# Kernel optimization log

Hardware: AMD Instinct MI355X
Metric: run time of the kernel (lower is better)

The kernel has to match this reference:

```python
import jax, jax.numpy as jnp
import numpy as np

B, C, H, W = 8, 512, 32, 32
NH, DH = 8, 64          # num_heads, head_dim (C = NH*DH)
GROUPS, EPS = 32, 1e-5


def group_norm(x, gamma, beta):
    b, c, h, w = x.shape
    xg = x.reshape(b, GROUPS, c // GROUPS, h, w)
    mu = xg.mean(axis=(2, 3, 4), keepdims=True)
    var = xg.var(axis=(2, 3, 4), keepdims=True)
    xn = ((xg - mu) * jax.lax.rsqrt(var + EPS)).reshape(b, c, h, w)
    return xn * gamma[:, None, None] + beta[:, None, None]


def conv1x1(x, w, b):
    # x: [B,C,H,W], w: [O,C], b: [O]
    return jnp.einsum('bchw,oc->bohw', x, w) + b[:, None, None]


def setup_inputs() -> dict:
    key = jax.random.key(0)
    ks = jax.random.split(key, 5)
    return {
        'x': jax.random.normal(ks[0], (B, C, H, W), jnp.float32),
        'norm_gamma': jnp.ones((C,), jnp.float32),
        'norm_beta': jnp.zeros((C,), jnp.float32),
        'qkv_w': jax.random.normal(ks[1], (3 * C, C), jnp.float32) * (1.0 / np.sqrt(C)),
        'qkv_b': jax.random.normal(ks[2], (3 * C,), jnp.float32) * 0.02,
        'proj_w': jax.random.normal(ks[3], (C, C), jnp.float32) * (1.0 / np.sqrt(C)),
        'proj_b': jax.random.normal(ks[4], (C,), jnp.float32) * 0.02,
    }


def reference(x, norm_gamma, norm_beta, qkv_w, qkv_b, proj_w, proj_b):
    scale = DH ** -0.5
    h = group_norm(x, norm_gamma, norm_beta)
    qkv = conv1x1(h, qkv_w, qkv_b)                       # [B,3C,H,W]
    qkv = qkv.reshape(B, 3, NH, DH, H * W)
    qkv = jnp.transpose(qkv, (1, 0, 2, 4, 3))            # [3,B,NH,HW,DH]
    q, k, v = qkv[0], qkv[1], qkv[2]
    attn = jnp.einsum('bhid,bhjd->bhij', q, k) * scale   # [B,NH,HW,HW]
    attn = jax.nn.softmax(attn, axis=-1)
    h = jnp.einsum('bhij,bhjd->bhid', attn, v)           # [B,NH,HW,DH]
    # faithful to torch: direct row-major reshape [B,NH,HW,DH] -> [B,C,H,W]
    h = h.reshape(B, C, H, W)
    h = conv1x1(h, proj_w, proj_b)
    return x + h
```

## Files before the change

### kernel.cpp

```cpp
#include <hip/hip_runtime.h>


typedef float  f32x4  __attribute__((ext_vector_type(4)));
typedef __bf16 bf16x8 __attribute__((ext_vector_type(8)));
typedef __bf16 bf16x4 __attribute__((ext_vector_type(4)));
typedef short  s16x4  __attribute__((ext_vector_type(4)));

#define MFMA(a, b, c) __builtin_amdgcn_mfma_f32_16x16x32_bf16(a, b, c, 0, 0, 0)
#define MFMA16(a, b, c) __builtin_amdgcn_mfma_f32_16x16x16bf16_1k( \
    __builtin_bit_cast(s16x4, a), __builtin_bit_cast(s16x4, b), c, 0, 0, 0)

__device__ __forceinline__ void async16(const __bf16* g, __bf16* l) {
  __builtin_amdgcn_global_load_lds((const __attribute__((address_space(1))) void*)g,
                                   (__attribute__((address_space(3))) void*)l, 16, 0, 0);
}

__device__ __forceinline__ int chk(int n, int c) {
  return ((((n >> 6) * 16 + (c >> 5)) * 4 + ((c >> 3) & 3)) * 512) + (n & 63) * 8 + (c & 7);
}

__global__ __launch_bounds__(512) void gn_cvt_k(const float* __restrict__ x,
                                                const float* __restrict__ gamma,
                                                const float* __restrict__ beta,
                                                __bf16* __restrict__ Hout,
                                                const float* __restrict__ qw, __bf16* __restrict__ dq,
                                                const float* __restrict__ pw, __bf16* __restrict__ dp) {
  const int tid = threadIdx.x;
  if (blockIdx.x >= 256) {
    int i = ((blockIdx.x - 256) * 512 + tid) * 4;
    const float* src = (i < 786432) ? qw : pw;
    __bf16* dst = (i < 786432) ? dq : dp;
    int j = (i < 786432) ? i : (i - 786432);
    int m = j >> 9, k = j & 511;
    float4 v = *(const float4*)(src + j);
    bf16x4 o;
    o[0] = (__bf16)v.x; o[1] = (__bf16)v.y; o[2] = (__bf16)v.z; o[3] = (__bf16)v.w;
    *(bf16x4*)(dst + chk(m, k)) = o;
    return;
  }
  __shared__ __bf16 xs[16 * 1032];
  __shared__ float  red[16];
  __shared__ float  ga[16], be[16], stat[2];
  const int w = tid >> 6, l = tid & 63;
  const int bg = blockIdx.x, b = bg >> 5, g = bg & 31, c0 = g * 16;
  const float* xg = x + b * 524288 + c0 * 1024;

  float sum = 0.f, sq = 0.f;
#pragma unroll
  for (int p = 0; p < 8; p++) {
    int idx = p * 2048 + tid * 4;
    float4 v = *(const float4*)(xg + idx);
    int c = idx >> 10, s = idx & 1023;
    bf16x4 o;
    o[0] = (__bf16)v.x; o[1] = (__bf16)v.y; o[2] = (__bf16)v.z; o[3] = (__bf16)v.w;
    *(bf16x4*)(&xs[c * 1032 + s]) = o;
    sum += v.x + v.y + v.z + v.w;
    sq  += v.x * v.x + v.y * v.y + v.z * v.z + v.w * v.w;
  }
#pragma unroll
  for (int o = 32; o > 0; o >>= 1) { sum += __shfl_down(sum, o); sq += __shfl_down(sq, o); }
  if (l == 0) { red[w * 2] = sum; red[w * 2 + 1] = sq; }
  __syncthreads();
  if (tid == 0) {
    float S = 0.f, Q = 0.f;
#pragma unroll
    for (int i = 0; i < 8; i++) { S += red[i * 2]; Q += red[i * 2 + 1]; }
    float mean = S * (1.f / 16384.f);
    float var  = Q * (1.f / 16384.f) - mean * mean;
    stat[0] = mean; stat[1] = rsqrtf(var + 1e-5f);
  }
  if (tid < 16) { ga[tid] = gamma[c0 + tid]; be[tid] = beta[c0 + tid]; }
  __syncthreads();
  const float mean = stat[0], rstd = stat[1];
#pragma unroll
  for (int p = 0; p < 2; p++) {
    int s = p * 512 + tid;
    int n = b * 1024 + s;
    bf16x8 o0, o1;
#pragma unroll
    for (int c = 0; c < 8; c++) {
      float f = (float)xs[c * 1032 + s];
      o0[c] = (__bf16)((f - mean) * rstd * ga[c] + be[c]);
    }
#pragma unroll
    for (int c = 8; c < 16; c++) {
      float f = (float)xs[c * 1032 + s];
      o1[c - 8] = (__bf16)((f - mean) * rstd * ga[c] + be[c]);
    }
    *(bf16x8*)(Hout + chk(n, c0)) = o0;
    *(bf16x8*)(Hout + chk(n, c0 + 8)) = o1;
  }
}

__global__ __launch_bounds__(256) void gemm_qkv_k(const __bf16* __restrict__ W,
                                                  const float* __restrict__ bias,
                                                  const __bf16* __restrict__ H,
                                                  __bf16* __restrict__ qbuf,
                                                  __bf16* __restrict__ kbuf,
                                                  __bf16* __restrict__ vt) {
  __shared__ union {
    struct { __bf16 a[2][4096]; __bf16 b[2][4096]; } ab;
    __bf16 cs[128 * 136];
  } lds;
  const int tid = threadIdx.x;
  const int w = tid >> 6, l = tid & 63, quad = l >> 4, li = l & 15;
  const int wr = w >> 1, wc = w & 1;
  const int mblk = blockIdx.x >> 6, nblk = blockIdx.x & 63;
  const int m0 = mblk * 128, n0 = nblk * 128;

  f32x4 acc[4][4];
#pragma unroll
  for (int i = 0; i < 4; i++)
#pragma unroll
    for (int j = 0; j < 4; j++) acc[i][j] = f32x4{0.f, 0.f, 0.f, 0.f};

  const __bf16* Ag = W + (((m0 >> 6) * 16) * 4 + w) * 512 + l * 8;
  const __bf16* Bg = H + (((n0 >> 6) * 16) * 4 + w) * 512 + l * 8;
  const int halfA = 16 * 4 * 512;

  async16(Ag,         &lds.ab.a[0][w * 1024]);
  async16(Ag + halfA, &lds.ab.a[0][w * 1024 + 512]);
  async16(Bg,         &lds.ab.b[0][w * 1024]);
  async16(Bg + halfA, &lds.ab.b[0][w * 1024 + 512]);

#pragma unroll 1
  for (int kt = 0; kt < 16; kt++) {
    int cur = kt & 1, nxt = cur ^ 1;
    __syncthreads();
    if (kt < 15) {
      int ko = (kt + 1) * 2048;
      async16(Ag + ko,          &lds.ab.a[nxt][w * 1024]);
      async16(Ag + halfA + ko,  &lds.ab.a[nxt][w * 1024 + 512]);
      async16(Bg + ko,          &lds.ab.b[nxt][w * 1024]);
      async16(Bg + halfA + ko,  &lds.ab.b[nxt][w * 1024 + 512]);
    }
    bf16x8 af[4], bfr[4];
#pragma unroll
    for (int i = 0; i < 4; i++)
      af[i] = *(const bf16x8*)(&lds.ab.a[cur][quad * 1024 + (wr * 64 + i * 16 + li) * 8]);
#pragma unroll
    for (int i = 0; i < 4; i++)
      bfr[i] = *(const bf16x8*)(&lds.ab.b[cur][quad * 1024 + (wc * 64 + i * 16 + li) * 8]);
#pragma unroll
    for (int i = 0; i < 4; i++)
#pragma unroll
      for (int j = 0; j < 4; j++) acc[i][j] = MFMA(af[i], bfr[j], acc[i][j]);
  }

  const int t = m0 >> 9;
  const int cbase = m0 & 511;
  __syncthreads();
#pragma unroll
  for (int mi = 0; mi < 4; mi++) {
    int olocal = wr * 64 + mi * 16 + quad * 4;
    float bs[4];
#pragma unroll
    for (int r = 0; r < 4; r++) bs[r] = bias[m0 + olocal + r];
#pragma unroll
    for (int ni = 0; ni < 4; ni++) {
      int nlocal = wc * 64 + ni * 16 + li;
      bf16x4 pk;
#pragma unroll
      for (int r = 0; r < 4; r++) {
        float f = acc[mi][ni][r] + bs[r];
        if (t == 0) f *= 0.180336880f;
        pk[r] = (__bf16)f;
      }
      *(bf16x4*)(&lds.cs[nlocal * 136 + olocal]) = pk;
    }
  }
  __syncthreads();
  const int bb = n0 >> 10, s0 = n0 & 1023;
  if (t < 2) {
    __bf16* dst = (t == 0) ? qbuf : kbuf;
    const int nh0 = cbase >> 6;
#pragma unroll
    for (int p = 0; p < 8; p++) {
      int idx = p * 256 + tid;
      int oc = idx & 15, nloc = idx >> 4;
      uint4 val = *(const uint4*)(&lds.cs[nloc * 136 + oc * 8]);
      int bh = bb * 8 + nh0 + (oc >> 3);
      int s = s0 + nloc, d0 = (oc & 7) * 8;
      *(uint4*)(dst + (((bh * 16 + (s >> 6)) * 8 + (d0 >> 3)) * 64 + (s & 63)) * 8) = val;
    }
  } else {
#pragma unroll
    for (int p = 0; p < 8; p++) {
      int idx = p * 256 + tid;
      int o = idx & 127, ng = idx >> 7;
      int c = cbase + o, nh2 = c >> 6, d = c & 63;
      int bh = bb * 8 + nh2;
      int j0 = s0 + ng * 8;
      bf16x8 vv;
#pragma unroll
      for (int jj = 0; jj < 8; jj++) vv[jj] = lds.cs[(ng * 8 + jj) * 136 + o];
      *(bf16x8*)(vt + (((bh * 16 + (j0 >> 6)) * 8 + ((j0 >> 3) & 7)) * 64 + d) * 8) = vv;
    }
  }
}

__global__ __launch_bounds__(256) void attn_k(const __bf16* __restrict__ qb,
                                              const __bf16* __restrict__ kb,
                                              const __bf16* __restrict__ vt,
                                              __bf16* __restrict__ pin) {
  __shared__ __bf16 KC[2][4096];
  __shared__ __bf16 VC[2][4096];
  __shared__ union { __bf16 q[4096]; __bf16 o[4096]; } PQ;
  const int tid = threadIdx.x;
  const int w = tid >> 6, l = tid & 63, quad = l >> 4, li = l & 15;
  const int x = blockIdx.x;
  const int qt = (x >> 3) & 15;
  const int bh = (x & 7) | ((x >> 7) << 3);
  const int b = bh >> 3, nh = bh & 7;
  const __bf16* Qg = qb + bh * 65536;
  const __bf16* Kg = kb + bh * 65536;
  const __bf16* Vg = vt + bh * 65536;

#pragma unroll
  for (int p = 0; p < 2; p++) {
    int ch = w + 4 * p;
    async16(Qg + ((qt * 8 + ch) * 64) * 8 + l * 8, &PQ.q[ch * 512 + l * 8]);
    async16(Kg + (ch * 64) * 8 + l * 8,            &KC[0][ch * 512 + l * 8]);
    async16(Vg + (ch * 64) * 8 + l * 8,            &VC[0][ch * 512 + l * 8]);
  }
  __syncthreads();
  bf16x8 qf[2];
#pragma unroll
  for (int ks = 0; ks < 2; ks++)
    qf[ks] = *(const bf16x8*)(&PQ.q[(ks * 4 + quad) * 512 + (w * 16 + li) * 8]);

  float lsum = 0.f;
  f32x4 oacc[4];
#pragma unroll
  for (int dt = 0; dt < 4; dt++) oacc[dt] = f32x4{0.f, 0.f, 0.f, 0.f};

#pragma unroll 1
  for (int kv = 0; kv < 16; kv++) {
    int cur = kv & 1, nxt = cur ^ 1;
    if (kv < 15) {
#pragma unroll
      for (int p = 0; p < 2; p++) {
        int ch = w + 4 * p;
        async16(Kg + (((kv + 1) * 8 + ch) * 64) * 8 + l * 8, &KC[nxt][ch * 512 + l * 8]);
        async16(Vg + (((kv + 1) * 8 + ch) * 64) * 8 + l * 8, &VC[nxt][ch * 512 + l * 8]);
      }
    }

    f32x4 st[4];
#pragma unroll
    for (int jt = 0; jt < 4; jt++) st[jt] = f32x4{0.f, 0.f, 0.f, 0.f};
#pragma unroll
    for (int ks = 0; ks < 2; ks++)
#pragma unroll
      for (int jt = 0; jt < 4; jt++) {
        bf16x8 kf = *(const bf16x8*)(&KC[cur][(ks * 4 + quad) * 512 + (jt * 16 + li) * 8]);
        st[jt] = MFMA(kf, qf[ks], st[jt]);
      }

#pragma unroll
    for (int jt = 0; jt < 4; jt++) {
      f32x4 v = st[jt];
      bf16x4 pk;
      float p0 = __builtin_amdgcn_exp2f(v[0]);
      float p1 = __builtin_amdgcn_exp2f(v[1]);
      float p2 = __builtin_amdgcn_exp2f(v[2]);
      float p3 = __builtin_amdgcn_exp2f(v[3]);
      lsum += (p0 + p1) + (p2 + p3);
      pk[0] = (__bf16)p0; pk[1] = (__bf16)p1; pk[2] = (__bf16)p2; pk[3] = (__bf16)p3;
      const int jbase = (jt * 2 + (quad >> 1)) * 512 + (quad & 1) * 4;
#pragma unroll
      for (int dt = 0; dt < 4; dt++) {
        bf16x4 vf = *(const bf16x4*)(&VC[cur][jbase + (dt * 16 + li) * 8]);
        oacc[dt] = MFMA16(pk, vf, oacc[dt]);
      }
    }
    __syncthreads();
  }

  lsum += __shfl_xor(lsum, 16);
  lsum += __shfl_xor(lsum, 32);
  const float inv = 1.f / lsum;
#pragma unroll
  for (int r = 0; r < 4; r++) {
    float ib = __shfl(inv, quad * 4 + r);
#pragma unroll
    for (int dt = 0; dt < 4; dt++)
      PQ.o[((quad * 4 + r) * 64 + dt * 16 + li) * 4 + w] = (__bf16)(oacc[dt][r] * ib);
  }
  __syncthreads();
  __bf16* Pg = pin + (nh * 8 + (qt >> 1)) * 65536 + (qt & 1) * 4 + b * 8192;
#pragma unroll
  for (int p = 0; p < 4; p++) {
    int n = p * 256 + tid;
    bf16x4 ov = *(const bf16x4*)(&PQ.o[n * 4]);
    *(bf16x4*)(Pg + n * 8) = ov;
  }
}

__global__ __launch_bounds__(256) void gemm_proj_k(const __bf16* __restrict__ W,
                                                   const float* __restrict__ bias,
                                                   const __bf16* __restrict__ P,
                                                   const float* __restrict__ x,
                                                   float* __restrict__ out) {
  __shared__ __bf16 AL[2][2048];
  __shared__ __bf16 BL[2][4096];
  const int tid = threadIdx.x;
  const int w = tid >> 6, l = tid & 63, quad = l >> 4, li = l & 15;
  const int wr = w >> 1, wc = w & 1;
  const int mblk = blockIdx.x >> 6, nblk = blockIdx.x & 63;
  const int m0 = mblk * 64, n0 = nblk * 128;

  f32x4 acc[2][4];
#pragma unroll
  for (int i = 0; i < 2; i++)
#pragma unroll
    for (int j = 0; j < 4; j++) acc[i][j] = f32x4{0.f, 0.f, 0.f, 0.f};

  const __bf16* Ag = W + ((mblk * 16) * 4 + w) * 512 + l * 8;
  const __bf16* Bg = P + w * 65536 + (n0 + l) * 8;

  async16(Ag,       &AL[0][w * 512]);
  async16(Bg,       &BL[0][w * 1024]);
  async16(Bg + 512, &BL[0][w * 1024 + 512]);

#pragma unroll 1
  for (int kt = 0; kt < 16; kt++) {
    int cur = kt & 1, nxt = cur ^ 1;
    __syncthreads();
    if (kt < 15) {
      int koA = (kt + 1) * 2048;
      int koB = (kt + 1) * 262144;
      async16(Ag + koA,       &AL[nxt][w * 512]);
      async16(Bg + koB,       &BL[nxt][w * 1024]);
      async16(Bg + koB + 512, &BL[nxt][w * 1024 + 512]);
    }
    bf16x8 af[2], bfr[4];
#pragma unroll
    for (int i = 0; i < 2; i++)
      af[i] = *(const bf16x8*)(&AL[cur][quad * 512 + (wr * 32 + i * 16 + li) * 8]);
#pragma unroll
    for (int j = 0; j < 4; j++)
      bfr[j] = *(const bf16x8*)(&BL[cur][quad * 1024 + (wc * 64 + j * 16 + li) * 8]);
#pragma unroll
    for (int i = 0; i < 2; i++)
#pragma unroll
      for (int j = 0; j < 4; j++) acc[i][j] = MFMA(af[i], bfr[j], acc[i][j]);
  }

  const int bb = n0 >> 10;
#pragma unroll
  for (int mi = 0; mi < 2; mi++) {
    int o = m0 + wr * 32 + mi * 16 + quad * 4;
    float bs[4];
#pragma unroll
    for (int r = 0; r < 4; r++) bs[r] = bias[o + r];
#pragma unroll
    for (int ni = 0; ni < 4; ni++) {
      int n = n0 + wc * 64 + ni * 16 + li;
      int s = n & 1023;
#pragma unroll
      for (int r = 0; r < 4; r++) {
        int a = (bb * 512 + o + r) * 1024 + s;
        out[a] = acc[mi][ni][r] + bs[r] + x[a];
      }
    }
  }
}

extern "C" void kernel_launch(void* const* d_in, const int* in_sizes, int n_in,
                              void* d_out, int out_size, void* d_ws, size_t ws_size,
                              hipStream_t stream) {
  const float* x      = (const float*)d_in[0];
  const float* gamma  = (const float*)d_in[1];
  const float* beta   = (const float*)d_in[2];
  const float* qkv_w  = (const float*)d_in[3];
  const float* qkv_b  = (const float*)d_in[4];
  const float* proj_w = (const float*)d_in[5];
  const float* proj_b = (const float*)d_in[6];

  __bf16* ws   = (__bf16*)d_ws;
  __bf16* H    = ws;
  __bf16* qbuf = ws + 4194304;
  __bf16* kbuf = ws + 8388608;
  __bf16* vt   = ws + 12582912;
  __bf16* wq   = ws + 16777216;
  __bf16* wp   = ws + 17563648;

  gn_cvt_k<<<768, 512, 0, stream>>>(x, gamma, beta, H, qkv_w, wq, proj_w, wp);
  gemm_qkv_k<<<768, 256, 0, stream>>>(wq, qkv_b, H, qbuf, kbuf, vt);
  attn_k<<<1024, 256, 0, stream>>>(qbuf, kbuf, vt, H);
  gemm_proj_k<<<512, 256, 0, stream>>>(wp, proj_b, H, x, (float*)d_out);
}
```

Baseline: 142.4 us.

## Split attention KV tiles across waves and reduce partial outputs through LDS

Each wave used to own 16 query rows and walk all 64 keys of every KV tile. Now each wave owns 16 keys of each tile and covers all 64 query rows, so K and V fragments are reused across four query sub-tiles. The partial outputs and row sums are then combined in a tree reduction through LDS, reusing the KV buffers, before normalising. This cuts LDS fragment reads per MFMA, but it raises register pressure (64 accumulator floats and 8 Q fragments per lane), adds a serial epilogue with several barriers, and lowers the launch-bounds occupancy hint to 3 blocks.

```diff
diff --git a/kernel.cpp b/kernel.cpp
--- a/kernel.cpp
+++ b/kernel.cpp
@@ -199,13 +199,14 @@
   }
 }
 
-__global__ __launch_bounds__(256) void attn_k(const __bf16* __restrict__ qb,
-                                              const __bf16* __restrict__ kb,
-                                              const __bf16* __restrict__ vt,
-                                              __bf16* __restrict__ pin) {
+__global__ __launch_bounds__(256, 3) void attn_k(const __bf16* __restrict__ qb,
+                                                 const __bf16* __restrict__ kb,
+                                                 const __bf16* __restrict__ vt,
+                                                 __bf16* __restrict__ pin) {
   __shared__ __bf16 KC[2][4096];
   __shared__ __bf16 VC[2][4096];
   __shared__ union { __bf16 q[4096]; __bf16 o[4096]; } PQ;
+  __shared__ float lred[128];
   const int tid = threadIdx.x;
   const int w = tid >> 6, l = tid & 63, quad = l >> 4, li = l & 15;
   const int x = blockIdx.x;
@@ -224,15 +225,19 @@
     async16(Vg + (ch * 64) * 8 + l * 8,            &VC[0][ch * 512 + l * 8]);
   }
   __syncthreads();
-  bf16x8 qf[2];
-#pragma unroll
-  for (int ks = 0; ks < 2; ks++)
-    qf[ks] = *(const bf16x8*)(&PQ.q[(ks * 4 + quad) * 512 + (w * 16 + li) * 8]);
-
-  float lsum = 0.f;
-  f32x4 oacc[4];
-#pragma unroll
-  for (int dt = 0; dt < 4; dt++) oacc[dt] = f32x4{0.f, 0.f, 0.f, 0.f};
+  bf16x8 qf[4][2];
+#pragma unroll
+  for (int it = 0; it < 4; it++)
+#pragma unroll
+    for (int ks = 0; ks < 2; ks++)
+      qf[it][ks] = *(const bf16x8*)(&PQ.q[(ks * 4 + quad) * 512 + (it * 16 + li) * 8]);
+
+  float lsum[4] = {0.f, 0.f, 0.f, 0.f};
+  f32x4 oacc[4][4];
+#pragma unroll
+  for (int it = 0; it < 4; it++)
+#pragma unroll
+    for (int dt = 0; dt < 4; dt++) oacc[it][dt] = f32x4{0.f, 0.f, 0.f, 0.f};
 
 #pragma unroll 1
   for (int kv = 0; kv < 16; kv++) {
@@ -248,44 +253,107 @@
 
     f32x4 st[4];
 #pragma unroll
-    for (int jt = 0; jt < 4; jt++) st[jt] = f32x4{0.f, 0.f, 0.f, 0.f};
-#pragma unroll
-    for (int ks = 0; ks < 2; ks++)
-#pragma unroll
-      for (int jt = 0; jt < 4; jt++) {
-        bf16x8 kf = *(const bf16x8*)(&KC[cur][(ks * 4 + quad) * 512 + (jt * 16 + li) * 8]);
-        st[jt] = MFMA(kf, qf[ks], st[jt]);
+    for (int it = 0; it < 4; it++) st[it] = f32x4{0.f, 0.f, 0.f, 0.f};
+#pragma unroll
+    for (int ks = 0; ks < 2; ks++) {
+      bf16x8 kf = *(const bf16x8*)(&KC[cur][(ks * 4 + quad) * 512 + (w * 16 + li) * 8]);
+#pragma unroll
+      for (int it = 0; it < 4; it++) st[it] = MFMA(kf, qf[it][ks], st[it]);
+    }
+
+    bf16x4 pk[4];
+#pragma unroll
+    for (int it = 0; it < 4; it++) {
+      float p0 = __builtin_amdgcn_exp2f(st[it][0]);
+      float p1 = __builtin_amdgcn_exp2f(st[it][1]);
+      float p2 = __builtin_amdgcn_exp2f(st[it][2]);
+      float p3 = __builtin_amdgcn_exp2f(st[it][3]);
+      lsum[it] += (p0 + p1) + (p2 + p3);
+      pk[it][0] = (__bf16)p0; pk[it][1] = (__bf16)p1;
+      pk[it][2] = (__bf16)p2; pk[it][3] = (__bf16)p3;
+    }
+    const int vbase = (w * 2 + (quad >> 1)) * 512 + (quad & 1) * 4;
+#pragma unroll
+    for (int dt = 0; dt < 4; dt++) {
+      bf16x4 vf = *(const bf16x4*)(&VC[cur][vbase + (dt * 16 + li) * 8]);
+#pragma unroll
+      for (int it = 0; it < 4; it++) oacc[it][dt] = MFMA16(pk[it], vf, oacc[it][dt]);
+    }
+    __syncthreads();
+  }
+
+#pragma unroll
+  for (int it = 0; it < 4; it++) {
+    lsum[it] += __shfl_xor(lsum[it], 16);
+    lsum[it] += __shfl_xor(lsum[it], 32);
+  }
+  float* const slot0 = (float*)&KC[0][0];
+  float* const slot1 = (float*)&VC[0][0];
+  if (w & 1) {
+    float* s = (w == 1) ? slot0 : slot1;
+#pragma unroll
+    for (int it = 0; it < 4; it++)
+#pragma unroll
+      for (int dt = 0; dt < 4; dt++)
+#pragma unroll
+        for (int r = 0; r < 4; r++)
+          s[(it * 16 + quad * 4 + r) * 64 + dt * 16 + li] = oacc[it][dt][r];
+    if (quad == 0) {
+      float* lr = &lred[(w == 1) ? 0 : 64];
+#pragma unroll
+      for (int it = 0; it < 4; it++) lr[it * 16 + li] = lsum[it];
+    }
+  }
+  __syncthreads();
+  if (!(w & 1)) {
+    const float* s = (w == 0) ? slot0 : slot1;
+#pragma unroll
+    for (int it = 0; it < 4; it++)
+#pragma unroll
+      for (int dt = 0; dt < 4; dt++)
+#pragma unroll
+        for (int r = 0; r < 4; r++)
+          oacc[it][dt][r] += s[(it * 16 + quad * 4 + r) * 64 + dt * 16 + li];
+    const float* lr = &lred[(w == 0) ? 0 : 64];
+#pragma unroll
+    for (int it = 0; it < 4; it++) lsum[it] += lr[it * 16 + li];
+  }
+  __syncthreads();
+  if (w == 2) {
+#pragma unroll
+    for (int it = 0; it < 4; it++)
+#pragma unroll
+      for (int dt = 0; dt < 4; dt++)
+#pragma unroll
+        for (int r = 0; r < 4; r++)
+          slot0[(it * 16 + quad * 4 + r) * 64 + dt * 16 + li] = oacc[it][dt][r];
+    if (quad == 0)
+#pragma unroll
+      for (int it = 0; it < 4; it++) lred[it * 16 + li] = lsum[it];
+  }
+  __syncthreads();
+  if (w == 0) {
+#pragma unroll
+    for (int it = 0; it < 4; it++) {
+#pragma unroll
+      for (int dt = 0; dt < 4; dt++)
+#pragma unroll
+        for (int r = 0; r < 4; r++)
+          oacc[it][dt][r] += slot0[(it * 16 + quad * 4 + r) * 64 + dt * 16 + li];
+      lsum[it] += lred[it * 16 + li];
+    }
+#pragma unroll
+    for (int it = 0; it < 4; it++) {
+      float inv = 1.f / lsum[it];
+#pragma unroll
+      for (int r = 0; r < 4; r++) {
+        float ib = __shfl(inv, quad * 4 + r);
+#pragma unroll
+        for (int dt = 0; dt < 4; dt++)
+          PQ.o[((quad * 4 + r) * 64 + dt * 16 + li) * 4 + it] =
+              (__bf16)(oacc[it][dt][r] * ib);
       }
-
-#pragma unroll
-    for (int jt = 0; jt < 4; jt++) {
-      f32x4 v = st[jt];
-      bf16x4 pk;
-      float p0 = __builtin_amdgcn_exp2f(v[0]);
-      float p1 = __builtin_amdgcn_exp2f(v[1]);
-      float p2 = __builtin_amdgcn_exp2f(v[2]);
-      float p3 = __builtin_amdgcn_exp2f(v[3]);
-      lsum += (p0 + p1) + (p2 + p3);
-      pk[0] = (__bf16)p0; pk[1] = (__bf16)p1; pk[2] = (__bf16)p2; pk[3] = (__bf16)p3;
-      const int jbase = (jt * 2 + (quad >> 1)) * 512 + (quad & 1) * 4;
-#pragma unroll
-      for (int dt = 0; dt < 4; dt++) {
-        bf16x4 vf = *(const bf16x4*)(&VC[cur][jbase + (dt * 16 + li) * 8]);
-        oacc[dt] = MFMA16(pk, vf, oacc[dt]);
-      }
-    }
-    __syncthreads();
-  }
-
-  lsum += __shfl_xor(lsum, 16);
-  lsum += __shfl_xor(lsum, 32);
-  const float inv = 1.f / lsum;
-#pragma unroll
-  for (int r = 0; r < 4; r++) {
-    float ib = __shfl(inv, quad * 4 + r);
-#pragma unroll
-    for (int dt = 0; dt < 4; dt++)
-      PQ.o[((quad * 4 + r) * 64 + dt * 16 + li) * 4 + w] = (__bf16)(oacc[dt][r] * ib);
+    }
   }
   __syncthreads();
   __bf16* Pg = pin + (nh * 8 + (qt >> 1)) * 65536 + (qt & 1) * 4 + b * 8192;
```

After: 148.2 us. 1.04x slower.

## Triple-buffer async LDS loads with vmcnt-gated barriers; P via LDS for 16x16x32 MFMA

Applied to the files above, without the earlier changes.

Converts the QKV GEMM, attention and projection GEMM main loops from double to triple buffering. Loads are issued two tiles ahead, and each iteration ends with a single barrier that waits only for the older tile's loads (a partial vmcnt), so more memory traffic overlaps compute. In attention, probabilities are staged through a per-wave LDS buffer so the PV product can use the wider 16x16x32 MFMA instead of 16x16x16. This raises LDS use per block, which may reduce occupancy, and adds LDS writes and reads for P.

```diff
diff --git a/kernel.cpp b/kernel.cpp
--- a/kernel.cpp
+++ b/kernel.cpp
@@ -4,11 +4,10 @@
 typedef float  f32x4  __attribute__((ext_vector_type(4)));
 typedef __bf16 bf16x8 __attribute__((ext_vector_type(8)));
 typedef __bf16 bf16x4 __attribute__((ext_vector_type(4)));
-typedef short  s16x4  __attribute__((ext_vector_type(4)));
 
 #define MFMA(a, b, c) __builtin_amdgcn_mfma_f32_16x16x32_bf16(a, b, c, 0, 0, 0)
-#define MFMA16(a, b, c) __builtin_amdgcn_mfma_f32_16x16x16bf16_1k( \
-    __builtin_bit_cast(s16x4, a), __builtin_bit_cast(s16x4, b), c, 0, 0, 0)
+
+#define PIPE_BARRIER(N) asm volatile("s_waitcnt lgkmcnt(0) vmcnt(" #N ")\n\ts_barrier" ::: "memory")
 
 __device__ __forceinline__ void async16(const __bf16* g, __bf16* l) {
   __builtin_amdgcn_global_load_lds((const __attribute__((address_space(1))) void*)g,
@@ -99,7 +98,7 @@
                                                   __bf16* __restrict__ kbuf,
                                                   __bf16* __restrict__ vt) {
   __shared__ union {
-    struct { __bf16 a[2][4096]; __bf16 b[2][4096]; } ab;
+    struct { __bf16 a[3][4096]; __bf16 b[3][4096]; } ab;
     __bf16 cs[128 * 136];
   } lds;
   const int tid = threadIdx.x;
@@ -118,33 +117,40 @@
   const __bf16* Bg = H + (((n0 >> 6) * 16) * 4 + w) * 512 + l * 8;
   const int halfA = 16 * 4 * 512;
 
-  async16(Ag,         &lds.ab.a[0][w * 1024]);
-  async16(Ag + halfA, &lds.ab.a[0][w * 1024 + 512]);
-  async16(Bg,         &lds.ab.b[0][w * 1024]);
-  async16(Bg + halfA, &lds.ab.b[0][w * 1024 + 512]);
-
+#pragma unroll
+  for (int kt = 0; kt < 2; kt++) {
+    int ko = kt * 2048;
+    async16(Ag + ko,          &lds.ab.a[kt][w * 1024]);
+    async16(Ag + halfA + ko,  &lds.ab.a[kt][w * 1024 + 512]);
+    async16(Bg + ko,          &lds.ab.b[kt][w * 1024]);
+    async16(Bg + halfA + ko,  &lds.ab.b[kt][w * 1024 + 512]);
+  }
+  PIPE_BARRIER(4);
+
+  int c0 = 0, c1 = 1, c2 = 2;
 #pragma unroll 1
   for (int kt = 0; kt < 16; kt++) {
-    int cur = kt & 1, nxt = cur ^ 1;
-    __syncthreads();
-    if (kt < 15) {
-      int ko = (kt + 1) * 2048;
-      async16(Ag + ko,          &lds.ab.a[nxt][w * 1024]);
-      async16(Ag + halfA + ko,  &lds.ab.a[nxt][w * 1024 + 512]);
-      async16(Bg + ko,          &lds.ab.b[nxt][w * 1024]);
-      async16(Bg + halfA + ko,  &lds.ab.b[nxt][w * 1024 + 512]);
+    if (kt < 14) {
+      int ko = (kt + 2) * 2048;
+      async16(Ag + ko,          &lds.ab.a[c2][w * 1024]);
+      async16(Ag + halfA + ko,  &lds.ab.a[c2][w * 1024 + 512]);
+      async16(Bg + ko,          &lds.ab.b[c2][w * 1024]);
+      async16(Bg + halfA + ko,  &lds.ab.b[c2][w * 1024 + 512]);
     }
     bf16x8 af[4], bfr[4];
 #pragma unroll
     for (int i = 0; i < 4; i++)
-      af[i] = *(const bf16x8*)(&lds.ab.a[cur][quad * 1024 + (wr * 64 + i * 16 + li) * 8]);
+      af[i] = *(const bf16x8*)(&lds.ab.a[c0][quad * 1024 + (wr * 64 + i * 16 + li) * 8]);
 #pragma unroll
     for (int i = 0; i < 4; i++)
-      bfr[i] = *(const bf16x8*)(&lds.ab.b[cur][quad * 1024 + (wc * 64 + i * 16 + li) * 8]);
+      bfr[i] = *(const bf16x8*)(&lds.ab.b[c0][quad * 1024 + (wc * 64 + i * 16 + li) * 8]);
 #pragma unroll
     for (int i = 0; i < 4; i++)
 #pragma unroll
       for (int j = 0; j < 4; j++) acc[i][j] = MFMA(af[i], bfr[j], acc[i][j]);
+    if (kt < 14)      PIPE_BARRIER(4);
+    else if (kt == 14) PIPE_BARRIER(0);
+    int t = c0; c0 = c1; c1 = c2; c2 = t;
   }
 
   const int t = m0 >> 9;
@@ -203,9 +209,10 @@
                                               const __bf16* __restrict__ kb,
                                               const __bf16* __restrict__ vt,
                                               __bf16* __restrict__ pin) {
-  __shared__ __bf16 KC[2][4096];
-  __shared__ __bf16 VC[2][4096];
-  __shared__ union { __bf16 q[4096]; __bf16 o[4096]; } PQ;
+  __shared__ __bf16 KC[3][4096];
+  __shared__ __bf16 VC[3][4096];
+  __shared__ __bf16 Qs[4096];
+  __shared__ __bf16 Ps[4096];
   const int tid = threadIdx.x;
   const int w = tid >> 6, l = tid & 63, quad = l >> 4, li = l & 15;
   const int x = blockIdx.x;
@@ -219,32 +226,45 @@
 #pragma unroll
   for (int p = 0; p < 2; p++) {
     int ch = w + 4 * p;
-    async16(Qg + ((qt * 8 + ch) * 64) * 8 + l * 8, &PQ.q[ch * 512 + l * 8]);
-    async16(Kg + (ch * 64) * 8 + l * 8,            &KC[0][ch * 512 + l * 8]);
-    async16(Vg + (ch * 64) * 8 + l * 8,            &VC[0][ch * 512 + l * 8]);
-  }
-  __syncthreads();
+    async16(Qg + ((qt * 8 + ch) * 64) * 8 + l * 8, &Qs[ch * 512 + l * 8]);
+  }
+#pragma unroll
+  for (int p = 0; p < 2; p++) {
+    int ch = w + 4 * p;
+    async16(Kg + (ch * 64) * 8 + l * 8, &KC[0][ch * 512 + l * 8]);
+    async16(Vg + (ch * 64) * 8 + l * 8, &VC[0][ch * 512 + l * 8]);
+  }
+#pragma unroll
+  for (int p = 0; p < 2; p++) {
+    int ch = w + 4 * p;
+    async16(Kg + ((8 + ch) * 64) * 8 + l * 8, &KC[1][ch * 512 + l * 8]);
+    async16(Vg + ((8 + ch) * 64) * 8 + l * 8, &VC[1][ch * 512 + l * 8]);
+  }
+  PIPE_BARRIER(4);
+
   bf16x8 qf[2];
 #pragma unroll
   for (int ks = 0; ks < 2; ks++)
-    qf[ks] = *(const bf16x8*)(&PQ.q[(ks * 4 + quad) * 512 + (w * 16 + li) * 8]);
+    qf[ks] = *(const bf16x8*)(&Qs[(ks * 4 + quad) * 512 + (w * 16 + li) * 8]);
 
   float lsum = 0.f;
   f32x4 oacc[4];
 #pragma unroll
   for (int dt = 0; dt < 4; dt++) oacc[dt] = f32x4{0.f, 0.f, 0.f, 0.f};
 
+  int c0 = 0, c1 = 1, c2 = 2;
 #pragma unroll 1
   for (int kv = 0; kv < 16; kv++) {
-    int cur = kv & 1, nxt = cur ^ 1;
-    if (kv < 15) {
+    if (kv < 14) {
 #pragma unroll
       for (int p = 0; p < 2; p++) {
         int ch = w + 4 * p;
-        async16(Kg + (((kv + 1) * 8 + ch) * 64) * 8 + l * 8, &KC[nxt][ch * 512 + l * 8]);
-        async16(Vg + (((kv + 1) * 8 + ch) * 64) * 8 + l * 8, &VC[nxt][ch * 512 + l * 8]);
+        async16(Kg + (((kv + 2) * 8 + ch) * 64) * 8 + l * 8, &KC[c2][ch * 512 + l * 8]);
+        async16(Vg + (((kv + 2) * 8 + ch) * 64) * 8 + l * 8, &VC[c2][ch * 512 + l * 8]);
       }
     }
+    const __bf16* KB = KC[c0];
+    const __bf16* VB = VC[c0];
 
     f32x4 st[4];
 #pragma unroll
@@ -253,7 +273,7 @@
     for (int ks = 0; ks < 2; ks++)
 #pragma unroll
       for (int jt = 0; jt < 4; jt++) {
-        bf16x8 kf = *(const bf16x8*)(&KC[cur][(ks * 4 + quad) * 512 + (jt * 16 + li) * 8]);
+        bf16x8 kf = *(const bf16x8*)(&KB[(ks * 4 + quad) * 512 + (jt * 16 + li) * 8]);
         st[jt] = MFMA(kf, qf[ks], st[jt]);
       }
 
@@ -267,32 +287,41 @@
       float p3 = __builtin_amdgcn_exp2f(v[3]);
       lsum += (p0 + p1) + (p2 + p3);
       pk[0] = (__bf16)p0; pk[1] = (__bf16)p1; pk[2] = (__bf16)p2; pk[3] = (__bf16)p3;
-      const int jbase = (jt * 2 + (quad >> 1)) * 512 + (quad & 1) * 4;
+      *(bf16x4*)(&Ps[w * 1024 + (jt * 2 + (quad >> 1)) * 128 + li * 8 + (quad & 1) * 4]) = pk;
+    }
+
+#pragma unroll
+    for (int ks2 = 0; ks2 < 2; ks2++) {
+      bf16x8 pf = *(const bf16x8*)(&Ps[w * 1024 + (ks2 * 4 + quad) * 128 + li * 8]);
 #pragma unroll
       for (int dt = 0; dt < 4; dt++) {
-        bf16x4 vf = *(const bf16x4*)(&VC[cur][jbase + (dt * 16 + li) * 8]);
-        oacc[dt] = MFMA16(pk, vf, oacc[dt]);
+        bf16x8 vf = *(const bf16x8*)(&VB[(ks2 * 4 + quad) * 512 + (dt * 16 + li) * 8]);
+        oacc[dt] = MFMA(pf, vf, oacc[dt]);
       }
     }
-    __syncthreads();
+
+    if (kv < 14)       PIPE_BARRIER(4);
+    else if (kv == 14) PIPE_BARRIER(0);
+    int t = c0; c0 = c1; c1 = c2; c2 = t;
   }
 
   lsum += __shfl_xor(lsum, 16);
   lsum += __shfl_xor(lsum, 32);
   const float inv = 1.f / lsum;
+  __syncthreads();
 #pragma unroll
   for (int r = 0; r < 4; r++) {
     float ib = __shfl(inv, quad * 4 + r);
 #pragma unroll
     for (int dt = 0; dt < 4; dt++)
-      PQ.o[((quad * 4 + r) * 64 + dt * 16 + li) * 4 + w] = (__bf16)(oacc[dt][r] * ib);
+      Ps[((quad * 4 + r) * 64 + dt * 16 + li) * 4 + w] = (__bf16)(oacc[dt][r] * ib);
   }
   __syncthreads();
   __bf16* Pg = pin + (nh * 8 + (qt >> 1)) * 65536 + (qt & 1) * 4 + b * 8192;
 #pragma unroll
   for (int p = 0; p < 4; p++) {
     int n = p * 256 + tid;
-    bf16x4 ov = *(const bf16x4*)(&PQ.o[n * 4]);
+    bf16x4 ov = *(const bf16x4*)(&Ps[n * 4]);
     *(bf16x4*)(Pg + n * 8) = ov;
   }
 }
@@ -302,8 +331,8 @@
                                                    const __bf16* __restrict__ P,
                                                    const float* __restrict__ x,
                                                    float* __restrict__ out) {
-  __shared__ __bf16 AL[2][2048];
-  __shared__ __bf16 BL[2][4096];
+  __shared__ __bf16 AL[3][2048];
+  __shared__ __bf16 BL[3][4096];
   const int tid = threadIdx.x;
   const int w = tid >> 6, l = tid & 63, quad = l >> 4, li = l & 15;
   const int wr = w >> 1, wc = w & 1;
@@ -319,32 +348,38 @@
   const __bf16* Ag = W + ((mblk * 16) * 4 + w) * 512 + l * 8;
   const __bf16* Bg = P + w * 65536 + (n0 + l) * 8;
 
-  async16(Ag,       &AL[0][w * 512]);
-  async16(Bg,       &BL[0][w * 1024]);
-  async16(Bg + 512, &BL[0][w * 1024 + 512]);
-
+#pragma unroll
+  for (int kt = 0; kt < 2; kt++) {
+    async16(Ag + kt * 2048,            &AL[kt][w * 512]);
+    async16(Bg + kt * 262144,          &BL[kt][w * 1024]);
+    async16(Bg + kt * 262144 + 512,    &BL[kt][w * 1024 + 512]);
+  }
+  PIPE_BARRIER(3);
+
+  int c0 = 0, c1 = 1, c2 = 2;
 #pragma unroll 1
   for (int kt = 0; kt < 16; kt++) {
-    int cur = kt & 1, nxt = cur ^ 1;
-    __syncthreads();
-    if (kt < 15) {
-      int koA = (kt + 1) * 2048;
-      int koB = (kt + 1) * 262144;
-      async16(Ag + koA,       &AL[nxt][w * 512]);
-      async16(Bg + koB,       &BL[nxt][w * 1024]);
-      async16(Bg + koB + 512, &BL[nxt][w * 1024 + 512]);
+    if (kt < 14) {
+      int koA = (kt + 2) * 2048;
+      int koB = (kt + 2) * 262144;
+      async16(Ag + koA,       &AL[c2][w * 512]);
+      async16(Bg + koB,       &BL[c2][w * 1024]);
+      async16(Bg + koB + 512, &BL[c2][w * 1024 + 512]);
     }
     bf16x8 af[2], bfr[4];
 #pragma unroll
     for (int i = 0; i < 2; i++)
-      af[i] = *(const bf16x8*)(&AL[cur][quad * 512 + (wr * 32 + i * 16 + li) * 8]);
+      af[i] = *(const bf16x8*)(&AL[c0][quad * 512 + (wr * 32 + i * 16 + li) * 8]);
 #pragma unroll
     for (int j = 0; j < 4; j++)
-      bfr[j] = *(const bf16x8*)(&BL[cur][quad * 1024 + (wc * 64 + j * 16 + li) * 8]);
+      bfr[j] = *(const bf16x8*)(&BL[c0][quad * 1024 + (wc * 64 + j * 16 + li) * 8]);
 #pragma unroll
     for (int i = 0; i < 2; i++)
 #pragma unroll
       for (int j = 0; j < 4; j++) acc[i][j] = MFMA(af[i], bfr[j], acc[i][j]);
+    if (kt < 14)       PIPE_BARRIER(3);
+    else if (kt == 14) PIPE_BARRIER(0);
+    int t = c0; c0 = c1; c1 = c2; c2 = t;
   }
 
   const int bb = n0 >> 10;
```

Result: slower. 149.6 us (+5.0%).
